# Performance work log

Hardware: AMD Instinct MI355X
Metric: run time of the kernel (lower is better)

The kernel has to match this reference:

```python
import jax, jax.numpy as jnp
import numpy as np

N = 20000   # nodes
E = 320000  # edges (avg degree 16)
F = 8       # n_original_features (tokens per node)
D = 16      # embed_dim
H = 4       # num_heads
OUT = 7     # classes


def setup_inputs() -> dict:
    key = jax.random.key(0)
    ks = jax.random.split(key, 12)
    s = 0.1
    return {
        "x": jax.random.normal(ks[0], (N, F * D), dtype=jnp.float32),
        "edge_index": jax.random.randint(ks[1], (2, E), 0, N, dtype=jnp.int32),
        "conv1_wqkv": jax.random.normal(ks[2], (3 * D, D), dtype=jnp.float32) * s,
        "conv1_bqkv": jnp.zeros((3 * D,), dtype=jnp.float32),
        "conv1_wo": jax.random.normal(ks[3], (D, D), dtype=jnp.float32) * s,
        "conv1_bo": jnp.zeros((D,), dtype=jnp.float32),
        "conv2_wqkv": jax.random.normal(ks[4], (3 * D, D), dtype=jnp.float32) * s,
        "conv2_bqkv": jnp.zeros((3 * D,), dtype=jnp.float32),
        "conv2_wo": jax.random.normal(ks[5], (D, D), dtype=jnp.float32) * s,
        "conv2_bo": jnp.zeros((D,), dtype=jnp.float32),
        "out_w": jax.random.normal(ks[6], (OUT, F * D), dtype=jnp.float32) * s,
        "out_b": jnp.zeros((OUT,), dtype=jnp.float32),
    }


def _mha_edge(xq, xkv, wqkv, bqkv, wo, bo):
    # xq, xkv: [E, F, D]. torch MultiheadAttention: query=xq, key=value=xkv.
    dh = D // H
    wq, wk, wv = jnp.split(wqkv, 3, axis=0)
    bq, bk, bv = jnp.split(bqkv, 3)
    q = (xq @ wq.T + bq).reshape(-1, F, H, dh)
    k = (xkv @ wk.T + bk).reshape(-1, F, H, dh)
    v = (xkv @ wv.T + bv).reshape(-1, F, H, dh)
    scale = 1.0 / np.sqrt(dh).astype(np.float32)
    scores = jnp.einsum('efhd,eghd->ehfg', q, k) * scale  # [E,H,F,F]
    attn = jax.nn.softmax(scores, axis=-1)
    out = jnp.einsum('ehfg,eghd->efhd', attn, v).reshape(-1, F, D)
    return out @ wo.T + bo


def _amp_conv(x, src, dst, wqkv, bqkv, wo, bo):
    # gather per-edge token views; query = target node tokens (x_i), key/value = source (x_j)
    xj = x[src].reshape(-1, F, D)
    xi = x[dst].reshape(-1, F, D)
    msg = _mha_edge(xi, xj, wqkv, bqkv, wo, bo).reshape(-1, F * D)
    return jax.ops.segment_sum(msg, dst, num_segments=N)  # aggr='add' at targets


def reference(x, edge_index, conv1_wqkv, conv1_bqkv, conv1_wo, conv1_bo,
              conv2_wqkv, conv2_bqkv, conv2_wo, conv2_bo, out_w, out_b):
    src, dst = edge_index[0], edge_index[1]
    h = _amp_conv(x, src, dst, conv1_wqkv, conv1_bqkv, conv1_wo, conv1_bo)
    h = jax.nn.elu(h)
    h = _amp_conv(h, src, dst, conv2_wqkv, conv2_bqkv, conv2_wo, conv2_bo)
    h = jax.nn.elu(h)
    logits = h @ out_w.T + out_b
    return jax.nn.log_softmax(logits, axis=1)
```

## Files before the change

kernel.cpp:

```cpp
#include <hip/hip_runtime.h>
#include <hip/hip_bf16.h>
#include <math.h>

#define NN 20000
#define NE 320000
#define FT 8
#define DM 16
#define FD 128
#define OUTC 7
#define NFD (NN * FD)

typedef unsigned short ushort;
typedef unsigned int uint;
typedef __fp16 h2 __attribute__((ext_vector_type(2)));
union UH { uint u; h2 h; };

__device__ inline h2 u2h(uint x) { UH c; c.u = x; return c.h; }

__device__ inline float dot2(uint a, h2 b, float c) {
#if __has_builtin(__builtin_amdgcn_fdot2)
    return __builtin_amdgcn_fdot2(u2h(a), b, c, false);
#else
    h2 ah = u2h(a);
    return fmaf((float)ah.x, (float)b.x, fmaf((float)ah.y, (float)b.y, c));
#endif
}
__device__ inline float dot2u(uint a, uint b, float c) { return dot2(a, u2h(b), c); }

__device__ inline h2 pk(float a, float b) {
#if __has_builtin(__builtin_amdgcn_cvt_pkrtz)
    return __builtin_amdgcn_cvt_pkrtz(a, b);
#else
    h2 r; r.x = (__fp16)a; r.y = (__fp16)b; return r;
#endif
}
__device__ inline ushort f16b(float x) {
    union { __fp16 h; ushort u; } c; c.h = (__fp16)x; return c.u;
}
__device__ inline float rcpf(float x) {
#if __has_builtin(__builtin_amdgcn_rcpf)
    return __builtin_amdgcn_rcpf(x);
#else
    return 1.0f / x;
#endif
}
__device__ inline float exp2r(float x) {
#if __has_builtin(__builtin_amdgcn_exp2f)
    return __builtin_amdgcn_exp2f(x);
#else
    return exp2f(x);
#endif
}

#define QSCALE 0.7213475204444817f


__global__ __launch_bounds__(256) void qkv1_kernel(
    const float* __restrict__ x,
    const float* __restrict__ wqkv, const float* __restrict__ bqkv,
    ushort* __restrict__ qout, ushort* __restrict__ kvout) {
    __shared__ float sw[48 * 17];
    __shared__ float sb[48];
    __shared__ float sx[2][FD];
    __shared__ uint squ[2][64];
    __shared__ uint skvu[2][128];
    const int t = threadIdx.x;
    const int nh = t >> 7, tl = t & 127;
    const int n = blockIdx.x * 2 + nh;
    for (int i = t; i < 48 * 16; i += 256) sw[(i >> 4) * 17 + (i & 15)] = wqkv[i];
    if (t < 48) sb[t] = bqkv[t];
    sx[nh][tl] = x[(size_t)n * FD + tl];
    __syncthreads();
    const int f = tl >> 4, d = tl & 15, h = d >> 2, dd = d & 3;
    float aq = sb[d], ak = sb[16 + d], av = sb[32 + d];
    const float* xr = &sx[nh][f * 16];
#pragma unroll
    for (int e = 0; e < 16; ++e) {
        const float xe = xr[e];
        aq = fmaf(xe, sw[d * 17 + e], aq);
        ak = fmaf(xe, sw[(16 + d) * 17 + e], ak);
        av = fmaf(xe, sw[(32 + d) * 17 + e], av);
    }
    ushort* sq = (ushort*)squ[nh];
    ushort* skv = (ushort*)skvu[nh];
    sq[tl] = f16b(aq * QSCALE);
    skv[h * 64 + f * 4 + dd] = f16b(ak);
    skv[h * 64 + 32 + dd * 8 + f] = f16b(av);
    __syncthreads();
    if (tl < 64) ((uint*)(qout + (size_t)n * FD))[tl] = squ[nh][tl];
    ((uint*)(kvout + (size_t)n * 256))[tl] = skvu[nh][tl];
}

__global__ __launch_bounds__(256) void deg_kernel(const int* __restrict__ dst,
                                                  int* __restrict__ deg) {
    const int e = blockIdx.x * 256 + threadIdx.x;
    if (e < NE) atomicAdd(&deg[dst[e]], 1);
}

__global__ __launch_bounds__(1024) void scan_kernel(const int* __restrict__ deg,
                                                    int* __restrict__ rowstart,
                                                    int* __restrict__ cursor) {
    __shared__ int wsum[16];
    __shared__ int s_carry;
    const int t = threadIdx.x;
    const int lane = t & 63, wid = t >> 6;
    if (t == 0) s_carry = 0;
    __syncthreads();
    for (int base = 0; base < NN; base += 1024) {
        const int i = base + t;
        const int d = (i < NN) ? deg[i] : 0;
        int s = d;
        for (int off = 1; off < 64; off <<= 1) {
            int tmp = __shfl_up(s, off);
            if (lane >= off) s += tmp;
        }
        if (lane == 63) wsum[wid] = s;
        __syncthreads();
        if (wid == 0) {
            int ws = (lane < 16) ? wsum[lane] : 0;
            for (int off = 1; off < 16; off <<= 1) {
                int tmp = __shfl_up(ws, off);
                if (lane >= off) ws += tmp;
            }
            if (lane < 16) wsum[lane] = ws;
        }
        __syncthreads();
        const int carry = s_carry;
        const int woff = (wid > 0) ? wsum[wid - 1] : 0;
        if (i < NN) {
            const int excl = carry + woff + s - d;
            rowstart[i] = excl;
            cursor[i] = excl;
        }
        __syncthreads();
        if (t == 1023) s_carry = carry + wsum[15];
        __syncthreads();
    }
    if (t == 0) rowstart[NN] = NE;
}

__global__ __launch_bounds__(256) void scatter_kernel(
    const int* __restrict__ src, const int* __restrict__ dst,
    int* __restrict__ cursor, int* __restrict__ csr_src) {
    const int e = blockIdx.x * 256 + threadIdx.x;
    if (e < NE) {
        const int pos = atomicAdd(&cursor[dst[e]], 1);
        csr_src[pos] = src[e];
    }
}

__global__ __launch_bounds__(256) void edge_agg_kernel(
    const int* __restrict__ rowstart, const int* __restrict__ csr_src,
    const ushort* __restrict__ qh, const uint* __restrict__ kvw,
    float* __restrict__ accum) {
    const int w = (blockIdx.x * 256 + threadIdx.x) >> 6;
    if (w >= NN) return;
    const int lane = threadIdx.x & 63;
    const int slot = lane >> 2;
    const int h    = lane & 3;

    const uint* qrow = (const uint*)(qh + (size_t)w * FD);
    uint2 qp[8];
#pragma unroll
    for (int f = 0; f < 8; ++f)
        qp[f] = *(const uint2*)(qrow + f * 8 + h * 2);

    const int beg = rowstart[w], end = rowstart[w + 1];

    float acc[8][4];
#pragma unroll
    for (int f = 0; f < 8; ++f)
#pragma unroll
        for (int dd = 0; dd < 4; ++dd) acc[f][dd] = 0.f;

    int e = beg + slot;
    uint idx = (e < end) ? (uint)csr_src[e] : 0u;
    float gate = (e < end) ? 1.0f : 0.0f;

    for (int eb = beg; eb < end; eb += 16) {
        const uint4* p = (const uint4*)(kvw + (size_t)idx * 128 + h * 32);
        const uint4 k0 = p[0], k1 = p[1], k2 = p[2], k3 = p[3];
        const uint4 v0 = p[4], v1 = p[5], v2 = p[6], v3 = p[7];
        const int en = eb + 16 + slot;
        const uint idxn = (en < end) ? (uint)csr_src[en] : 0u;
        const float gaten = (en < end) ? 1.0f : 0.0f;

#pragma unroll
        for (int f = 0; f < 8; ++f) {
            const uint qx = qp[f].x, qy = qp[f].y;
            float s0 = dot2u(qy, k0.y, dot2u(qx, k0.x, 0.f));
            float s1 = dot2u(qy, k0.w, dot2u(qx, k0.z, 0.f));
            float s2 = dot2u(qy, k1.y, dot2u(qx, k1.x, 0.f));
            float s3 = dot2u(qy, k1.w, dot2u(qx, k1.z, 0.f));
            float s4 = dot2u(qy, k2.y, dot2u(qx, k2.x, 0.f));
            float s5 = dot2u(qy, k2.w, dot2u(qx, k2.z, 0.f));
            float s6 = dot2u(qy, k3.y, dot2u(qx, k3.x, 0.f));
            float s7 = dot2u(qy, k3.w, dot2u(qx, k3.z, 0.f));
            s0 = exp2r(s0); s1 = exp2r(s1); s2 = exp2r(s2); s3 = exp2r(s3);
            s4 = exp2r(s4); s5 = exp2r(s5); s6 = exp2r(s6); s7 = exp2r(s7);
            const float sum = ((s0 + s1) + (s2 + s3)) + ((s4 + s5) + (s6 + s7));
            const float inv = gate * rcpf(sum);
            const h2 e0 = pk(s0, s1), e1 = pk(s2, s3), e2 = pk(s4, s5), e3 = pk(s6, s7);
            const float p0 = dot2(v0.w, e3, dot2(v0.z, e2, dot2(v0.y, e1, dot2(v0.x, e0, 0.f))));
            const float p1 = dot2(v1.w, e3, dot2(v1.z, e2, dot2(v1.y, e1, dot2(v1.x, e0, 0.f))));
            const float p2 = dot2(v2.w, e3, dot2(v2.z, e2, dot2(v2.y, e1, dot2(v2.x, e0, 0.f))));
            const float p3 = dot2(v3.w, e3, dot2(v3.z, e2, dot2(v3.y, e1, dot2(v3.x, e0, 0.f))));
            acc[f][0] = fmaf(p0, inv, acc[f][0]);
            acc[f][1] = fmaf(p1, inv, acc[f][1]);
            acc[f][2] = fmaf(p2, inv, acc[f][2]);
            acc[f][3] = fmaf(p3, inv, acc[f][3]);
        }
        idx = idxn; gate = gaten;
    }

#pragma unroll
    for (int f = 0; f < 8; ++f)
#pragma unroll
        for (int dd = 0; dd < 4; ++dd) {
            float a = acc[f][dd];
            a += __shfl_xor(a, 4);
            a += __shfl_xor(a, 8);
            a += __shfl_xor(a, 16);
            a += __shfl_xor(a, 32);
            acc[f][dd] = a;
        }
    if (slot == 0) {
        float* arow = accum + (size_t)w * FD;
#pragma unroll
        for (int f = 0; f < 8; ++f)
            *(float4*)(arow + f * 16 + h * 4) =
                make_float4(acc[f][0], acc[f][1], acc[f][2], acc[f][3]);
    }
}

__global__ __launch_bounds__(256) void post_qkv_kernel(
    const float* __restrict__ accum, const int* __restrict__ deg,
    const float* __restrict__ wo, const float* __restrict__ bo,
    const float* __restrict__ wqkv, const float* __restrict__ bqkv,
    ushort* __restrict__ qout, ushort* __restrict__ kvout) {
    __shared__ float swo[16 * 17];
    __shared__ float sbo[16];
    __shared__ float swq[48 * 17];
    __shared__ float sbq[48];
    __shared__ float sa[2][FD];
    __shared__ float sh[2][FD];
    __shared__ uint squ[2][64];
    __shared__ uint skvu[2][128];
    const int t = threadIdx.x;
    const int nh = t >> 7, tl = t & 127;
    const int n = blockIdx.x * 2 + nh;
    for (int i = t; i < 16 * 16; i += 256) swo[(i >> 4) * 17 + (i & 15)] = wo[i];
    for (int i = t; i < 48 * 16; i += 256) swq[(i >> 4) * 17 + (i & 15)] = wqkv[i];
    if (t < 16) sbo[t] = bo[t];
    if (t < 48) sbq[t] = bqkv[t];
    sa[nh][tl] = accum[(size_t)n * FD + tl];
    __syncthreads();
    const int f = tl >> 4, d = tl & 15, h = d >> 2, dd = d & 3;
    float hv = (float)deg[n] * sbo[d];
#pragma unroll
    for (int e = 0; e < 16; ++e) hv = fmaf(sa[nh][f * 16 + e], swo[d * 17 + e], hv);
    hv = hv > 0.f ? hv : expm1f(hv);
    sh[nh][tl] = hv;
    __syncthreads();
    float aq = sbq[d], ak = sbq[16 + d], av = sbq[32 + d];
    const float* xr = &sh[nh][f * 16];
#pragma unroll
    for (int e = 0; e < 16; ++e) {
        const float xe = xr[e];
        aq = fmaf(xe, swq[d * 17 + e], aq);
        ak = fmaf(xe, swq[(16 + d) * 17 + e], ak);
        av = fmaf(xe, swq[(32 + d) * 17 + e], av);
    }
    ushort* sq = (ushort*)squ[nh];
    ushort* skv = (ushort*)skvu[nh];
    sq[tl] = f16b(aq * QSCALE);
    skv[h * 64 + f * 4 + dd] = f16b(ak);
    skv[h * 64 + 32 + dd * 8 + f] = f16b(av);
    __syncthreads();
    if (tl < 64) ((uint*)(qout + (size_t)n * FD))[tl] = squ[nh][tl];
    ((uint*)(kvout + (size_t)n * 256))[tl] = skvu[nh][tl];
}

__global__ __launch_bounds__(256) void post_cls_kernel(
    const float* __restrict__ accum, const int* __restrict__ deg,
    const float* __restrict__ wo, const float* __restrict__ bo,
    const float* __restrict__ cw, const float* __restrict__ cb,
    float* __restrict__ out) {
    __shared__ float swo[16 * 17];
    __shared__ float sbo[16];
    __shared__ float scw[OUTC * FD];
    __shared__ float sa[2][FD];
    __shared__ float sred[2][2][OUTC];
    const int t = threadIdx.x;
    const int nh = t >> 7, tl = t & 127;
    const int n = blockIdx.x * 2 + nh;
    for (int i = t; i < 16 * 16; i += 256) swo[(i >> 4) * 17 + (i & 15)] = wo[i];
    for (int i = t; i < OUTC * FD; i += 256) scw[i] = cw[i];
    if (t < 16) sbo[t] = bo[t];
    sa[nh][tl] = accum[(size_t)n * FD + tl];
    __syncthreads();
    const int f = tl >> 4, d = tl & 15;
    const int lane = t & 63, wid = (t >> 6) & 1;
    float hv = (float)deg[n] * sbo[d];
#pragma unroll
    for (int e = 0; e < 16; ++e) hv = fmaf(sa[nh][f * 16 + e], swo[d * 17 + e], hv);
    hv = hv > 0.f ? hv : expm1f(hv);
    float p[OUTC];
#pragma unroll
    for (int c = 0; c < OUTC; ++c) p[c] = hv * scw[c * FD + tl];
#pragma unroll
    for (int c = 0; c < OUTC; ++c)
        for (int off = 32; off; off >>= 1) p[c] += __shfl_xor(p[c], off);
    if (lane == 0)
#pragma unroll
        for (int c = 0; c < OUTC; ++c) sred[nh][wid][c] = p[c];
    __syncthreads();
    if (tl == 0) {
        float lg[OUTC];
        float m = -1e30f;
#pragma unroll
        for (int c = 0; c < OUTC; ++c) {
            lg[c] = sred[nh][0][c] + sred[nh][1][c] + cb[c];
            m = fmaxf(m, lg[c]);
        }
        float s = 0.f;
#pragma unroll
        for (int c = 0; c < OUTC; ++c) s += __expf(lg[c] - m);
        const float lse = m + logf(s);
#pragma unroll
        for (int c = 0; c < OUTC; ++c) out[(size_t)n * OUTC + c] = lg[c] - lse;
    }
}

extern "C" void kernel_launch(void* const* d_in, const int* in_sizes, int n_in,
                              void* d_out, int out_size, void* d_ws, size_t ws_size,
                              hipStream_t stream) {
    const float* x      = (const float*)d_in[0];
    const int*   ei     = (const int*)d_in[1];
    const float* w1qkv  = (const float*)d_in[2];
    const float* b1qkv  = (const float*)d_in[3];
    const float* w1o    = (const float*)d_in[4];
    const float* b1o    = (const float*)d_in[5];
    const float* w2qkv  = (const float*)d_in[6];
    const float* b2qkv  = (const float*)d_in[7];
    const float* w2o    = (const float*)d_in[8];
    const float* b2o    = (const float*)d_in[9];
    const float* outw   = (const float*)d_in[10];
    const float* outb   = (const float*)d_in[11];
    float* out = (float*)d_out;

    const int* srcp = ei;
    const int* dstp = ei + NE;

    ushort* qh    = (ushort*)d_ws;
    ushort* kvh   = qh + (size_t)NN * FD;
    float*  accum = (float*)(kvh + (size_t)NN * 256);
    int*    deg      = (int*)(accum + NFD);
    int*    rowstart = deg + NN;
    int*    cursor   = rowstart + NN + 1;
    int*    csr_src  = cursor + NN;

    (void)hipMemsetAsync(deg, 0, NN * sizeof(int), stream);
    deg_kernel<<<(NE + 255) / 256, 256, 0, stream>>>(dstp, deg);
    scan_kernel<<<1, 1024, 0, stream>>>(deg, rowstart, cursor);
    scatter_kernel<<<(NE + 255) / 256, 256, 0, stream>>>(srcp, dstp, cursor, csr_src);

    qkv1_kernel<<<NN / 2, 256, 0, stream>>>(x, w1qkv, b1qkv, qh, kvh);
    edge_agg_kernel<<<NN / 4, 256, 0, stream>>>(rowstart, csr_src, qh, (const uint*)kvh, accum);
    post_qkv_kernel<<<NN / 2, 256, 0, stream>>>(accum, deg, w1o, b1o, w2qkv, b2qkv, qh, kvh);
    edge_agg_kernel<<<NN / 4, 256, 0, stream>>>(rowstart, csr_src, qh, (const uint*)kvh, accum);
    post_cls_kernel<<<NN / 2, 256, 0, stream>>>(accum, deg, w2o, b2o, outw, outb, out);
}
```

Baseline: 228.4 us.

## Sort nodes into degree bins so edge aggregation wavefronts balance work

Adds a histogram, a bin scan and a ballot-based scatter that build a node permutation grouped by degree class. The edge aggregation kernel then maps each wavefront to a node through this permutation, so waves in the same block handle nodes of similar degree. This targets load imbalance from variable node degree. It costs three extra small kernel launches plus an indirect lookup, and nodes within a bin are ordered non-deterministically, which can hurt locality of the output writes.

After: 393.7 us. 1.72x slower.

```diff
diff --git a/kernel.cpp b/kernel.cpp
--- a/kernel.cpp
+++ b/kernel.cpp
@@ -9,6 +9,7 @@
 #define FD 128
 #define OUTC 7
 #define NFD (NN * FD)
+#define NBIN 8
 
 typedef unsigned short ushort;
 typedef unsigned int uint;
@@ -149,12 +150,55 @@
     }
 }
 
+__device__ inline int degclass(int d) {
+    int b = (d + 15) >> 4;
+    return b < NBIN - 1 ? b : NBIN - 1;
+}
+
+__global__ __launch_bounds__(256) void hist_kernel(const int* __restrict__ deg,
+                                                   int* __restrict__ bins) {
+    const int n = blockIdx.x * 256 + threadIdx.x;
+    if (n < NN) atomicAdd(&bins[degclass(deg[n])], 1);
+}
+
+__global__ __launch_bounds__(64) void binscan_kernel(const int* __restrict__ bins,
+                                                     int* __restrict__ bincur) {
+    if (threadIdx.x == 0) {
+        int acc = 0;
+        for (int b = 0; b < NBIN; ++b) { bincur[b] = acc; acc += bins[b]; }
+    }
+}
+
+__global__ __launch_bounds__(256) void permscatter_kernel(
+    const int* __restrict__ deg, int* __restrict__ bincur,
+    int* __restrict__ perm) {
+    const int n = blockIdx.x * 256 + threadIdx.x;
+    const int lane = threadIdx.x & 63;
+    const bool valid = n < NN;
+    const int b = valid ? degclass(deg[n]) : -1;
+    for (int bb = 0; bb < NBIN; ++bb) {
+        const unsigned long long mask = __ballot(b == bb);
+        if (mask) {
+            const int leader = __ffsll((long long)mask) - 1;
+            int base = 0;
+            if (lane == leader) base = atomicAdd(&bincur[bb], __popcll(mask));
+            base = __shfl(base, leader);
+            if (b == bb) {
+                const int rank = __popcll(mask & ((1ull << lane) - 1ull));
+                perm[base + rank] = n;
+            }
+        }
+    }
+}
+
 __global__ __launch_bounds__(256) void edge_agg_kernel(
     const int* __restrict__ rowstart, const int* __restrict__ csr_src,
+    const int* __restrict__ perm,
     const ushort* __restrict__ qh, const uint* __restrict__ kvw,
     float* __restrict__ accum) {
-    const int w = (blockIdx.x * 256 + threadIdx.x) >> 6;
-    if (w >= NN) return;
+    const int wid = (blockIdx.x * 256 + threadIdx.x) >> 6;
+    if (wid >= NN) return;
+    const int w = perm[wid];
     const int lane = threadIdx.x & 63;
     const int slot = lane >> 2;
     const int h    = lane & 3;
@@ -356,18 +400,24 @@
     ushort* kvh   = qh + (size_t)NN * FD;
     float*  accum = (float*)(kvh + (size_t)NN * 256);
     int*    deg      = (int*)(accum + NFD);
-    int*    rowstart = deg + NN;
+    int*    bins     = deg + NN;
+    int*    rowstart = bins + NBIN;
     int*    cursor   = rowstart + NN + 1;
-    int*    csr_src  = cursor + NN;
-
-    (void)hipMemsetAsync(deg, 0, NN * sizeof(int), stream);
+    int*    bincur   = cursor + NN;
+    int*    perm     = bincur + NBIN;
+    int*    csr_src  = perm + NN;
+
+    (void)hipMemsetAsync(deg, 0, (NN + NBIN) * sizeof(int), stream);
     deg_kernel<<<(NE + 255) / 256, 256, 0, stream>>>(dstp, deg);
+    hist_kernel<<<(NN + 255) / 256, 256, 0, stream>>>(deg, bins);
     scan_kernel<<<1, 1024, 0, stream>>>(deg, rowstart, cursor);
+    binscan_kernel<<<1, 64, 0, stream>>>(bins, bincur);
+    permscatter_kernel<<<(NN + 255) / 256, 256, 0, stream>>>(deg, bincur, perm);
     scatter_kernel<<<(NE + 255) / 256, 256, 0, stream>>>(srcp, dstp, cursor, csr_src);
 
     qkv1_kernel<<<NN / 2, 256, 0, stream>>>(x, w1qkv, b1qkv, qh, kvh);
-    edge_agg_kernel<<<NN / 4, 256, 0, stream>>>(rowstart, csr_src, qh, (const uint*)kvh, accum);
+    edge_agg_kernel<<<NN / 4, 256, 0, stream>>>(rowstart, csr_src, perm, qh, (const uint*)kvh, accum);
     post_qkv_kernel<<<NN / 2, 256, 0, stream>>>(accum, deg, w1o, b1o, w2qkv, b2qkv, qh, kvh);
-    edge_agg_kernel<<<NN / 4, 256, 0, stream>>>(rowstart, csr_src, qh, (const uint*)kvh, accum);
+    edge_agg_kernel<<<NN / 4, 256, 0, stream>>>(rowstart, csr_src, perm, qh, (const uint*)kvh, accum);
     post_cls_kernel<<<NN / 2, 256, 0, stream>>>(accum, deg, w2o, b2o, outw, outb, out);
 }
```
